# Performance work log

Measured on AMD Instinct MI355X. Metric: run time of the kernel, lower is better.

Reference implementation:

```python
import jax, jax.numpy as jnp
import numpy as np

NUM_ITERS = 2  # quasi-DEER fixed-point iterations (module default num_iters=2)


def _affine_scan(A, b):
    """Parallel first-order linear recurrence h_t = A_t*h_{t-1} + b_t along axis=1.
    A, b: (B, T, H). Equivalent to torch accelerated-scan after removing pow-2 padding."""
    def comb(l, r):
        A1, b1 = l
        A2, b2 = r
        return A2 * A1, A2 * b1 + b2
    return jax.lax.associative_scan(comb, (A, b), axis=1)[1]


def _run_direction(x, W_in, b_in, W_rec, U_z, b_u, num_iters):
    """quasi-DEER evaluation of a MinRNN layer.
    x: (B, T, d_in). Returns states (B, T, H). Initial state h0 = 0 (hx=None)."""
    B, T, _ = x.shape
    H = b_in.shape[0]
    dtype = x.dtype
    h0 = jnp.zeros((B, H), dtype)
    diag_rec = jnp.diagonal(W_rec)  # (H,)
    # z depends only on the input, not on the state -> precompute once.
    z = jnp.tanh(jnp.einsum('bti,hi->bth', x, W_in) + b_in)  # (B, T, H)
    z0, z_rest = z[:, 0], z[:, 1:]
    states = jnp.zeros((B, T, H), dtype)
    for _ in range(num_iters):
        h_prev = states[:, :-1]  # (B, T-1, H), paired with inputs[:,1:]
        u = jax.nn.sigmoid(jnp.einsum('bth,gh->btg', h_prev, W_rec)
                           + jnp.einsum('bth,gh->btg', z_rest, U_z) + b_u)
        fs = u * h_prev + (1.0 - u) * z_rest                      # cell output f
        As = u + (h_prev - z_rest) * u * (1.0 - u) * diag_rec     # diagonal Jacobian
        bs = fs - As * h_prev
        u0 = jax.nn.sigmoid(h0 @ W_rec.T + z0 @ U_z.T + b_u)
        b0 = u0 * h0 + (1.0 - u0) * z0                            # f(x_0, h0)
        A = jnp.concatenate([jnp.zeros_like(b0)[:, None], As], axis=1)  # A0 = 0
        b = jnp.concatenate([b0[:, None], bs], axis=1)
        states = _affine_scan(A, b)
    return states


def _prnn_forward(input, Wf_in, bf_in, Wf_rec, Uf_z, bf_u,
                  Wb_in, bb_in, Wb_rec, Ub_z, bb_u):
    fwd = _run_direction(input, Wf_in, bf_in, Wf_rec, Uf_z, bf_u, NUM_ITERS)
    bwd = _run_direction(input[:, ::-1], Wb_in, bb_in, Wb_rec, Ub_z, bb_u, NUM_ITERS)[:, ::-1]
    output = jnp.concatenate([fwd, bwd], axis=2)      # (B, T, 2H)
    h_n = jnp.stack([fwd[:, -1], bwd[:, 0]])          # (2, B, H)
    return output, h_n


def setup_inputs() -> dict:
    key = jax.random.key(0)
    ks = jax.random.split(key, 12)
    B, T, D_IN, H = 8, 8192, 256, 256
    def minrnn_params(k0, k1, k2, d_in, h):
        kw, kr, ku = k0, k1, k2
        return dict(
            W_in=jax.random.normal(kw, (h, d_in), jnp.float32) / d_in ** 0.5,
            b_in=jnp.zeros((h,), jnp.float32),
            W_rec=jax.random.normal(kr, (h, h), jnp.float32) / h ** 0.5,
            U_z=jax.random.normal(ku, (h, h), jnp.float32) / h ** 0.5,
            b_u=jnp.zeros((h,), jnp.float32),
        )
    pf = minrnn_params(ks[0], ks[1], ks[2], D_IN, H)
    pb = minrnn_params(ks[3], ks[4], ks[5], D_IN, H)
    return {
        'input': jax.random.normal(ks[6], (B, T, D_IN), jnp.float32),
        'Wf_in': pf['W_in'], 'bf_in': pf['b_in'], 'Wf_rec': pf['W_rec'],
        'Uf_z': pf['U_z'], 'bf_u': pf['b_u'],
        'Wb_in': pb['W_in'], 'bb_in': pb['b_in'], 'Wb_rec': pb['W_rec'],
        'Ub_z': pb['U_z'], 'bb_u': pb['b_u'],
    }


def reference(input, Wf_in, bf_in, Wf_rec, Uf_z, bf_u,
              Wb_in, bb_in, Wb_rec, Ub_z, bb_u):
    return _prnn_forward(input, Wf_in, bf_in, Wf_rec, Uf_z, bf_u,
                         Wb_in, bb_in, Wb_rec, Ub_z, bb_u)
```

## Files before the change

### kernel.cpp

```cpp
#include <hip/hip_runtime.h>
#include <stdint.h>

typedef unsigned short u16;
typedef __attribute__((ext_vector_type(8))) short short8v;
typedef __attribute__((ext_vector_type(4))) short short4v;
typedef __attribute__((ext_vector_type(4))) float f32x4;

#define B_ 8
#define T_ 8192
#define H_ 256
#define M_ 65536
#define MH 16777216
#define NCH 256
#define CHL 32
#define NCHAN 4096

__device__ __forceinline__ u16 f2bf(float f) {
  union { float f; uint32_t u; } v; v.f = f;
  return (u16)((v.u + 0x7FFFu + ((v.u >> 16) & 1u)) >> 16);
}
__device__ __forceinline__ float bf2f(u16 s) {
  union { uint32_t u; float f; } v; v.u = ((uint32_t)s) << 16;
  return v.f;
}
__device__ __forceinline__ float sigm(float x) {
  return __fdividef(1.0f, 1.0f + __expf(-x));
}
__device__ __forceinline__ float tanhfast(float x) {
  return 1.0f - __fdividef(2.0f, __expf(2.0f * x) + 1.0f);
}

__global__ __launch_bounds__(256) void prep_kernel(
    const float* __restrict__ x, u16* __restrict__ xf,
    const float* __restrict__ w0, const float* __restrict__ w1, const float* __restrict__ w2,
    const float* __restrict__ w3, const float* __restrict__ w4, const float* __restrict__ w5,
    u16* __restrict__ wbf) {
  const int bx = blockIdx.x;
  const float* src;
  u16* dst;
  size_t i;
  if (bx < 8192) {
    i = ((size_t)bx * 256 + threadIdx.x) * 8;
    src = x; dst = xf;
  } else {
    const int r = bx - 8192;
    const int wsel = r >> 5, blk = r & 31;
    src = (wsel == 0) ? w0 : (wsel == 1) ? w1 : (wsel == 2) ? w2
        : (wsel == 3) ? w3 : (wsel == 4) ? w4 : w5;
    dst = wbf + (size_t)wsel * 65536;
    i = ((size_t)blk * 256 + threadIdx.x) * 8;
  }
  const float4* s4 = (const float4*)(src + i);
  float4 a = s4[0], b = s4[1];
  short8v o;
  o[0] = (short)f2bf(a.x); o[1] = (short)f2bf(a.y);
  o[2] = (short)f2bf(a.z); o[3] = (short)f2bf(a.w);
  o[4] = (short)f2bf(b.x); o[5] = (short)f2bf(b.y);
  o[6] = (short)f2bf(b.z); o[7] = (short)f2bf(b.w);
  *(short8v*)(dst + i) = o;
}

__device__ __forceinline__ void g2l16(const void* g, void* l) {
  __builtin_amdgcn_global_load_lds((const __attribute__((address_space(1))) void*)g,
                                   (__attribute__((address_space(3))) void*)l, 16, 0, 0);
}

template <int EPI, int REVZ>
__global__ __launch_bounds__(256) void gemm_k(const u16* __restrict__ A, size_t strideA,
                                              const u16* __restrict__ Bw,
                                              const float* __restrict__ bias0,
                                              const float* __restrict__ bias1,
                                              const u16* addm, u16* C) {
  __shared__ __align__(16) char lds[32768];
  char* ldsA = lds;
  char* ldsB = lds + 16384;
  const int bz = blockIdx.z;
  A += (size_t)bz * strideA;
  Bw += (size_t)bz * 196608;
  C += (size_t)bz * (size_t)MH;
  if (EPI == 3) addm += (size_t)bz * (size_t)MH;
  const float* bias = bz ? bias1 : bias0;

  const int tid = threadIdx.x;
  const int l = tid & 63, w = tid >> 6;
  const int tm = blockIdx.x, tn = blockIdx.y;
  const int m0 = (w >> 1) * 64, n0 = (w & 1) * 64;
  const int wbase = w * 1024;
  const bool rev = REVZ && (bz == 1);

  f32x4 vzero = {0.f, 0.f, 0.f, 0.f};
  f32x4 acc[4][4];
#pragma unroll
  for (int i = 0; i < 4; ++i)
#pragma unroll
    for (int j = 0; j < 4; ++j) acc[i][j] = vzero;

#pragma unroll
  for (int k0 = 0; k0 < 256; k0 += 64) {
#pragma unroll
    for (int is = 0; is < 4; ++is) {
      const int o = is * 4096 + tid * 16;
      const int row = o >> 7;
      const int cb = o & 127;
      int rA = tm * 128 + row;
      if (rev) { int bb = rA >> 13; int t = rA & 8191; rA = (bb << 13) + (8191 - t); }
      const char* gA = (const char*)A + (size_t)rA * 512 + k0 * 2 + cb;
      g2l16(gA, ldsA + is * 4096 + wbase);
      const int rB = tn * 128 + row;
      const char* gB = (const char*)Bw + (size_t)rB * 512 + k0 * 2 + cb;
      g2l16(gB, ldsB + is * 4096 + wbase);
    }
    __syncthreads();
#pragma unroll
    for (int ks = 0; ks < 2; ++ks) {
      short8v av[4], bv[4];
#pragma unroll
      for (int i = 0; i < 4; ++i) {
        av[i] = *(const short8v*)(ldsA + (m0 + i * 16 + (l & 15)) * 128 + ks * 64 + (l >> 4) * 16);
        bv[i] = *(const short8v*)(ldsB + (n0 + i * 16 + (l & 15)) * 128 + ks * 64 + (l >> 4) * 16);
      }
#pragma unroll
      for (int i = 0; i < 4; ++i)
#pragma unroll
        for (int j = 0; j < 4; ++j)
          acc[i][j] = __builtin_amdgcn_mfma_f32_16x16x32_bf16(av[i], bv[j], acc[i][j], 0, 0, 0);
    }
    __syncthreads();
  }

  u16* lt = (u16*)lds;
  const int colL = n0 + (l & 15);
  const int rowL0 = m0 + ((l >> 4) << 2);
#pragma unroll
  for (int j = 0; j < 4; ++j) {
    const int cl = colL + j * 16;
    const int cg = tn * 128 + cl;
    const float bv = (EPI == 3) ? 0.f : bias[cg];
#pragma unroll
    for (int i = 0; i < 4; ++i)
#pragma unroll
      for (int r = 0; r < 4; ++r) {
        const int rl = rowL0 + i * 16 + r;
        float xv = acc[i][j][r] + bv;
        if (EPI == 3) xv += bf2f(addm[(size_t)(tm * 128 + rl) * 256 + cg]);
        if (EPI == 0) xv = tanhfast(xv);
        lt[rl * 128 + cl] = f2bf(xv);
      }
  }
  __syncthreads();
#pragma unroll
  for (int itr = 0; itr < 8; ++itr) {
    const int rl = w * 32 + itr * 4 + (l >> 4);
    const int cb = (l & 15) * 16;
    short8v v = *(const short8v*)((const char*)lt + rl * 256 + cb);
    *(short8v*)((char*)C + (size_t)(tm * 128 + rl) * 512 + tn * 256 + cb) = v;
  }
}

__device__ __forceinline__ void compute_Ab(float zf, float ag, float hp, float dr,
                                           float& Aa, float& bb) {
  const float u = sigm(ag);
  const float g = u * (1.f - u) * dr;
  Aa = u + (hp - zf) * g;
  bb = u * hp + (1.f - u) * zf - Aa * hp;
}

template <int ITER>
__global__ __launch_bounds__(256) void scan_p1_kernel(
    const u16* __restrict__ zb, const u16* __restrict__ zub,
    const u16* __restrict__ s1b,
    const float* __restrict__ Wf_rec, const float* __restrict__ Wb_rec,
    float* __restrict__ P, float* __restrict__ q) {
  const int wid = blockIdx.x * 4 + (threadIdx.x >> 6);
  const int lane = threadIdx.x & 63;
  const int c = wid & (NCH - 1);
  const int tmp = wid >> 8;
  const int b = tmp & 7;
  const int d = tmp >> 3;
  const int h0 = lane * 4;
  const float* Wr = d ? Wb_rec : Wf_rec;
  float dr[4];
#pragma unroll
  for (int j = 0; j < 4; ++j) dr[j] = Wr[(h0 + j) * 257];
  const size_t off = (size_t)d * MH + ((size_t)b * T_ + (size_t)c * CHL) * H_ + h0;
  const u16* zp = zb + off;
  const u16* zup = zub + off;
  const u16* s1p = s1b + off;
  float Pv[4] = {1.f, 1.f, 1.f, 1.f}, qv[4] = {0.f, 0.f, 0.f, 0.f};
#pragma unroll 4
  for (int it = 0; it < CHL; ++it) {
    const size_t ix = (size_t)it * H_;
    short4v z4 = *(const short4v*)(zp + ix);
    short4v a4 = *(const short4v*)(zup + ix);
    short4v s4 = {0, 0, 0, 0};
    if (ITER == 2) s4 = *(const short4v*)(s1p + ix);
#pragma unroll
    for (int j = 0; j < 4; ++j) {
      const float zf = bf2f((u16)z4[j]);
      const float ag = bf2f((u16)a4[j]);
      const float hp = (ITER == 2) ? bf2f((u16)s4[j]) : 0.f;
      float Aa, bb;
      compute_Ab(zf, ag, hp, dr[j], Aa, bb);
      qv[j] = Aa * qv[j] + bb;
      Pv[j] *= Aa;
    }
  }
  const int ch0 = (d * 8 + b) * 256 + h0;
  *(f32x4*)(P + (size_t)c * NCHAN + ch0) = (f32x4){Pv[0], Pv[1], Pv[2], Pv[3]};
  *(f32x4*)(q + (size_t)c * NCHAN + ch0) = (f32x4){qv[0], qv[1], qv[2], qv[3]};
}

__global__ __launch_bounds__(256) void scan_p2_kernel(const float* __restrict__ P,
                                                      const float* __restrict__ q,
                                                      float* __restrict__ hstart) {
  const int ch = blockIdx.x * 256 + threadIdx.x;
  float hs = 0.f;
#pragma unroll 8
  for (int c = 0; c < NCH; ++c) {
    hstart[c * NCHAN + ch] = hs;
    hs = P[c * NCHAN + ch] * hs + q[c * NCHAN + ch];
  }
}

template <int ITER>
__global__ __launch_bounds__(256) void scan_p3_kernel(
    const u16* __restrict__ zb, const u16* __restrict__ zub,
    const u16* __restrict__ s1b,
    const float* __restrict__ Wf_rec, const float* __restrict__ Wb_rec,
    const float* __restrict__ hstart,
    u16* __restrict__ s1out, float* __restrict__ out, float* __restrict__ hn) {
  const int wid = blockIdx.x * 4 + (threadIdx.x >> 6);
  const int lane = threadIdx.x & 63;
  const int c = wid & (NCH - 1);
  const int tmp = wid >> 8;
  const int b = tmp & 7;
  const int d = tmp >> 3;
  const int h0 = lane * 4;
  const float* Wr = d ? Wb_rec : Wf_rec;
  float dr[4];
#pragma unroll
  for (int j = 0; j < 4; ++j) dr[j] = Wr[(h0 + j) * 257];
  const size_t off = (size_t)d * MH + ((size_t)b * T_ + (size_t)c * CHL) * H_ + h0;
  const u16* zp = zb + off;
  const u16* zup = zub + off;
  const u16* s1p = s1b + off;
  const int ch0 = (d * 8 + b) * 256 + h0;
  f32x4 h4 = *(const f32x4*)(hstart + (size_t)c * NCHAN + ch0);
  float hc[4] = {h4[0], h4[1], h4[2], h4[3]};
  if (ITER == 1 && c == 0) {
    *(short4v*)(s1out + off) = (short4v){0, 0, 0, 0};
  }
#pragma unroll 4
  for (int it = 0; it < CHL; ++it) {
    const size_t ix = (size_t)it * H_;
    short4v z4 = *(const short4v*)(zp + ix);
    short4v a4 = *(const short4v*)(zup + ix);
    short4v s4 = {0, 0, 0, 0};
    if (ITER == 2) s4 = *(const short4v*)(s1p + ix);
#pragma unroll
    for (int j = 0; j < 4; ++j) {
      const float zf = bf2f((u16)z4[j]);
      const float ag = bf2f((u16)a4[j]);
      const float hp = (ITER == 2) ? bf2f((u16)s4[j]) : 0.f;
      float Aa, bb;
      compute_Ab(zf, ag, hp, dr[j], Aa, bb);
      hc[j] = Aa * hc[j] + bb;
    }
    const int t = c * CHL + it;
    if (ITER == 1) {
      if (t < T_ - 1) {
        short4v o = {(short)f2bf(hc[0]), (short)f2bf(hc[1]),
                     (short)f2bf(hc[2]), (short)f2bf(hc[3])};
        *(short4v*)(s1out + off + ix + H_) = o;
      }
    } else {
      const size_t to = (d == 0) ? ((size_t)b * T_ + t) * 512 + h0
                                 : ((size_t)b * T_ + (T_ - 1 - t)) * 512 + 256 + h0;
      *(f32x4*)(out + to) = (f32x4){hc[0], hc[1], hc[2], hc[3]};
      if (t == T_ - 1)
        *(f32x4*)(hn + (size_t)(d * 8 + b) * 256 + h0) = (f32x4){hc[0], hc[1], hc[2], hc[3]};
    }
  }
}

extern "C" void kernel_launch(void* const* d_in, const int* in_sizes, int n_in,
                              void* d_out, int out_size, void* d_ws, size_t ws_size,
                              hipStream_t stream) {
  const float* x      = (const float*)d_in[0];
  const float* Wf_in  = (const float*)d_in[1];
  const float* bf_in  = (const float*)d_in[2];
  const float* Wf_rec = (const float*)d_in[3];
  const float* Uf_z   = (const float*)d_in[4];
  const float* bf_u   = (const float*)d_in[5];
  const float* Wb_in  = (const float*)d_in[6];
  const float* bb_in  = (const float*)d_in[7];
  const float* Wb_rec = (const float*)d_in[8];
  const float* Ub_z   = (const float*)d_in[9];
  const float* bb_u   = (const float*)d_in[10];

  char* ws = (char*)d_ws;
  const size_t BF = 33554432;
  u16* xf  = (u16*)(ws + 0 * BF);
  u16* z0  = (u16*)(ws + 1 * BF);
  u16* zu0 = (u16*)(ws + 3 * BF);
  u16* s10 = (u16*)(ws + 5 * BF);
  u16* wbf = (u16*)(ws + 7 * BF);
  char* pb = ws + 7 * BF + 1048576;
  float* Pbuf = (float*)(pb);
  float* qbuf = (float*)(pb + 4194304);
  float* hst  = (float*)(pb + 8388608);
  (void)ws_size; (void)in_sizes; (void)n_in; (void)out_size;

  float* outp = (float*)d_out;
  float* hnp  = outp + (size_t)33554432;

  dim3 gg(512, 2, 2);

  prep_kernel<<<8384, 256, 0, stream>>>(x, xf, Wf_in, Uf_z, Wf_rec, Wb_in, Ub_z, Wb_rec, wbf);

  gemm_k<0, 1><<<gg, 256, 0, stream>>>(xf, 0, wbf + 0 * 65536, bf_in, bb_in, nullptr, z0);
  gemm_k<1, 0><<<gg, 256, 0, stream>>>(z0, MH, wbf + 1 * 65536, bf_u, bb_u, nullptr, zu0);

  scan_p1_kernel<1><<<1024, 256, 0, stream>>>(z0, zu0, s10, Wf_rec, Wb_rec, Pbuf, qbuf);
  scan_p2_kernel<<<16, 256, 0, stream>>>(Pbuf, qbuf, hst);
  scan_p3_kernel<1><<<1024, 256, 0, stream>>>(z0, zu0, s10, Wf_rec, Wb_rec, hst,
                                              s10, nullptr, nullptr);

  gemm_k<3, 0><<<gg, 256, 0, stream>>>(s10, MH, wbf + 2 * 65536, nullptr, nullptr, zu0, zu0);

  scan_p1_kernel<2><<<1024, 256, 0, stream>>>(z0, zu0, s10, Wf_rec, Wb_rec, Pbuf, qbuf);
  scan_p2_kernel<<<16, 256, 0, stream>>>(Pbuf, qbuf, hst);
  scan_p3_kernel<2><<<1024, 256, 0, stream>>>(z0, zu0, s10, Wf_rec, Wb_rec, hst,
                                              nullptr, outp, hnp);
}
```

Before: 372.8 us.

## Fuse chunked scan phase-1 reduction into GEMM epilogues

Removes the separate scan_p1 kernels and computes each chunk's affine-scan products (P, q) inside the epilogue of the gate GEMMs, reading the gate pre-activations straight from LDS instead of re-reading them from global memory. Each GEMM tile of 128 rows covers four 32-step chunks and 128 hidden channels, and each thread scans two chunks serially. This saves one full read pass over the gate tensor plus two kernel launches. In exchange the GEMM epilogue grows longer and serialized, it issues scalar strided global loads for z and h, and the LDS reads across rows may cause bank conflicts.

```diff
diff --git a/kernel.cpp b/kernel.cpp
--- a/kernel.cpp
+++ b/kernel.cpp
@@ -28,6 +28,14 @@
 }
 __device__ __forceinline__ float tanhfast(float x) {
   return 1.0f - __fdividef(2.0f, __expf(2.0f * x) + 1.0f);
+}
+
+__device__ __forceinline__ void compute_Ab(float zf, float ag, float hp, float dr,
+                                           float& Aa, float& bb) {
+  const float u = sigm(ag);
+  const float g = u * (1.f - u) * dr;
+  Aa = u + (hp - zf) * g;
+  bb = u * hp + (1.f - u) * zf - Aa * hp;
 }
 
 __global__ __launch_bounds__(256) void prep_kernel(
@@ -65,12 +73,17 @@
                                    (__attribute__((address_space(3))) void*)l, 16, 0, 0);
 }
 
-template <int EPI, int REVZ>
+template <int EPI, int REVZ, int FUSE>
 __global__ __launch_bounds__(256) void gemm_k(const u16* __restrict__ A, size_t strideA,
                                               const u16* __restrict__ Bw,
                                               const float* __restrict__ bias0,
                                               const float* __restrict__ bias1,
-                                              const u16* addm, u16* C) {
+                                              const u16* addm, u16* C,
+                                              const u16* zp_g,
+                                              const float* __restrict__ Wf_rec,
+                                              const float* __restrict__ Wb_rec,
+                                              float* __restrict__ Pout,
+                                              float* __restrict__ qout) {
   __shared__ __align__(16) char lds[32768];
   char* ldsA = lds;
   char* ldsB = lds + 16384;
@@ -79,6 +92,7 @@
   Bw += (size_t)bz * 196608;
   C += (size_t)bz * (size_t)MH;
   if (EPI == 3) addm += (size_t)bz * (size_t)MH;
+  if (FUSE == 2) zp_g += (size_t)bz * (size_t)MH;
   const float* bias = bz ? bias1 : bias0;
 
   const int tid = threadIdx.x;
@@ -155,59 +169,34 @@
     short8v v = *(const short8v*)((const char*)lt + rl * 256 + cb);
     *(short8v*)((char*)C + (size_t)(tm * 128 + rl) * 512 + tn * 256 + cb) = v;
   }
-}
-
-__device__ __forceinline__ void compute_Ab(float zf, float ag, float hp, float dr,
-                                           float& Aa, float& bb) {
-  const float u = sigm(ag);
-  const float g = u * (1.f - u) * dr;
-  Aa = u + (hp - zf) * g;
-  bb = u * hp + (1.f - u) * zf - Aa * hp;
-}
-
-template <int ITER>
-__global__ __launch_bounds__(256) void scan_p1_kernel(
-    const u16* __restrict__ zb, const u16* __restrict__ zub,
-    const u16* __restrict__ s1b,
-    const float* __restrict__ Wf_rec, const float* __restrict__ Wb_rec,
-    float* __restrict__ P, float* __restrict__ q) {
-  const int wid = blockIdx.x * 4 + (threadIdx.x >> 6);
-  const int lane = threadIdx.x & 63;
-  const int c = wid & (NCH - 1);
-  const int tmp = wid >> 8;
-  const int b = tmp & 7;
-  const int d = tmp >> 3;
-  const int h0 = lane * 4;
-  const float* Wr = d ? Wb_rec : Wf_rec;
-  float dr[4];
-#pragma unroll
-  for (int j = 0; j < 4; ++j) dr[j] = Wr[(h0 + j) * 257];
-  const size_t off = (size_t)d * MH + ((size_t)b * T_ + (size_t)c * CHL) * H_ + h0;
-  const u16* zp = zb + off;
-  const u16* zup = zub + off;
-  const u16* s1p = s1b + off;
-  float Pv[4] = {1.f, 1.f, 1.f, 1.f}, qv[4] = {0.f, 0.f, 0.f, 0.f};
+
+  if (FUSE) {
+    const int cl = tid & 127;
+    const int hg = tn * 128 + cl;
+    const float dr = (bz ? Wb_rec : Wf_rec)[hg * 257];
+    const int bb = (tm * 128) >> 13;
+    const int c0 = ((tm * 128) & 8191) >> 5;
+    const int ch = (bz * 8 + bb) * 256 + hg;
+#pragma unroll
+    for (int cc = 0; cc < 2; ++cc) {
+      const int clc = (tid >> 7) * 2 + cc;
+      float Pv = 1.f, qv = 0.f;
+      const size_t gbase = (size_t)(tm * 128 + clc * CHL) * 256 + hg;
 #pragma unroll 4
-  for (int it = 0; it < CHL; ++it) {
-    const size_t ix = (size_t)it * H_;
-    short4v z4 = *(const short4v*)(zp + ix);
-    short4v a4 = *(const short4v*)(zup + ix);
-    short4v s4 = {0, 0, 0, 0};
-    if (ITER == 2) s4 = *(const short4v*)(s1p + ix);
-#pragma unroll
-    for (int j = 0; j < 4; ++j) {
-      const float zf = bf2f((u16)z4[j]);
-      const float ag = bf2f((u16)a4[j]);
-      const float hp = (ITER == 2) ? bf2f((u16)s4[j]) : 0.f;
-      float Aa, bb;
-      compute_Ab(zf, ag, hp, dr[j], Aa, bb);
-      qv[j] = Aa * qv[j] + bb;
-      Pv[j] *= Aa;
-    }
-  }
-  const int ch0 = (d * 8 + b) * 256 + h0;
-  *(f32x4*)(P + (size_t)c * NCHAN + ch0) = (f32x4){Pv[0], Pv[1], Pv[2], Pv[3]};
-  *(f32x4*)(q + (size_t)c * NCHAN + ch0) = (f32x4){qv[0], qv[1], qv[2], qv[3]};
+      for (int it = 0; it < CHL; ++it) {
+        const float ag = bf2f(lt[(clc * CHL + it) * 128 + cl]);
+        float zf, hp;
+        if (FUSE == 1) { zf = bf2f(A[gbase + (size_t)it * 256]); hp = 0.f; }
+        else { zf = bf2f(zp_g[gbase + (size_t)it * 256]); hp = bf2f(A[gbase + (size_t)it * 256]); }
+        float Aa, bbv;
+        compute_Ab(zf, ag, hp, dr, Aa, bbv);
+        qv = Aa * qv + bbv;
+        Pv *= Aa;
+      }
+      Pout[(size_t)(c0 + clc) * NCHAN + ch] = Pv;
+      qout[(size_t)(c0 + clc) * NCHAN + ch] = qv;
+    }
+  }
 }
 
 __global__ __launch_bounds__(256) void scan_p2_kernel(const float* __restrict__ P,
@@ -318,17 +307,21 @@
 
   prep_kernel<<<8384, 256, 0, stream>>>(x, xf, Wf_in, Uf_z, Wf_rec, Wb_in, Ub_z, Wb_rec, wbf);
 
-  gemm_k<0, 1><<<gg, 256, 0, stream>>>(xf, 0, wbf + 0 * 65536, bf_in, bb_in, nullptr, z0);
-  gemm_k<1, 0><<<gg, 256, 0, stream>>>(z0, MH, wbf + 1 * 65536, bf_u, bb_u, nullptr, zu0);
-
-  scan_p1_kernel<1><<<1024, 256, 0, stream>>>(z0, zu0, s10, Wf_rec, Wb_rec, Pbuf, qbuf);
+  gemm_k<0, 1, 0><<<gg, 256, 0, stream>>>(xf, 0, wbf + 0 * 65536, bf_in, bb_in,
+                                          nullptr, z0, nullptr, nullptr, nullptr,
+                                          nullptr, nullptr);
+  gemm_k<1, 0, 1><<<gg, 256, 0, stream>>>(z0, MH, wbf + 1 * 65536, bf_u, bb_u,
+                                          nullptr, zu0, nullptr, Wf_rec, Wb_rec,
+                                          Pbuf, qbuf);
+
   scan_p2_kernel<<<16, 256, 0, stream>>>(Pbuf, qbuf, hst);
   scan_p3_kernel<1><<<1024, 256, 0, stream>>>(z0, zu0, s10, Wf_rec, Wb_rec, hst,
                                               s10, nullptr, nullptr);
 
-  gemm_k<3, 0><<<gg, 256, 0, stream>>>(s10, MH, wbf + 2 * 65536, nullptr, nullptr, zu0, zu0);
-
-  scan_p1_kernel<2><<<1024, 256, 0, stream>>>(z0, zu0, s10, Wf_rec, Wb_rec, Pbuf, qbuf);
+  gemm_k<3, 0, 2><<<gg, 256, 0, stream>>>(s10, MH, wbf + 2 * 65536, nullptr, nullptr,
+                                          zu0, zu0, z0, Wf_rec, Wb_rec,
+                                          Pbuf, qbuf);
+
   scan_p2_kernel<<<16, 256, 0, stream>>>(Pbuf, qbuf, hst);
   scan_p3_kernel<2><<<1024, 256, 0, stream>>>(z0, zu0, s10, Wf_rec, Wb_rec, hst,
                                               nullptr, outp, hnp);
```

New measurement: 330.5 us. 1.13x faster.
